# Performance work log

Measured on AMD Instinct MI355X. Metric: run time of the kernel, lower is better.

## Reference

```python
import jax, jax.numpy as jnp
import numpy as np

B, H, W, DIM = 8, 128, 128, 96
MED = 2 * DIM            # med_channels
NS = 3                   # num_scales
SCTX = 48                # spatial context channels
RIN = DIM + SCTX         # reweight mlp input
RHID = int(0.25 * RIN)   # 36
ROUT = NS * MED          # 576
FH, FWH = H, W // 2 + 1  # rfft2 output grid
SCALE_HW = [(16, 9), (8, 4), (24, 13)]  # per-scale filter resolutions


def _cubic(t, a=-0.75):
    t = abs(t)
    if t <= 1.0:
        return (a + 2) * t ** 3 - (a + 3) * t ** 2 + 1.0
    if t < 2.0:
        return a * t ** 3 - 5 * a * t ** 2 + 8 * a * t - 4 * a
    return 0.0


def _resize_mat(old, new):
    # bicubic, align_corners=True, border replication (matches F.interpolate)
    M = np.zeros((new, old), dtype=np.float32)
    for j in range(new):
        s = j * (old - 1) / (new - 1) if new > 1 else 0.0
        f = int(np.floor(s))
        for k in range(-1, 3):
            M[j, min(max(f + k, 0), old - 1)] += _cubic(s - (f + k))
    return jnp.asarray(M)


def _soa(x, scale, bias):
    r = jnp.maximum(x, 0.0)
    return scale * r * r + bias


def setup_inputs() -> dict:
    key = jax.random.key(0)
    ks = jax.random.split(key, 10)
    inp = {
        "x": jax.random.normal(ks[0], (B, H, W, DIM), dtype=jnp.float32),
        "w1": jax.random.normal(ks[1], (MED, DIM), dtype=jnp.float32) * 0.02,
        "soa1_scale": jnp.ones((1,), jnp.float32),
        "soa1_bias": jnp.zeros((1,), jnp.float32),
        "cw0": jax.random.normal(ks[2], (SCALE_HW[0][0], SCALE_HW[0][1], MED, 2), dtype=jnp.float32) * 0.02,
        "cw1": jax.random.normal(ks[3], (SCALE_HW[1][0], SCALE_HW[1][1], MED, 2), dtype=jnp.float32) * 0.02,
        "cw2": jax.random.normal(ks[4], (SCALE_HW[2][0], SCALE_HW[2][1], MED, 2), dtype=jnp.float32) * 0.02,
        "sp_w": jax.random.normal(ks[5], (SCTX, DIM), dtype=jnp.float32) * 0.05,
        "bn_gamma": jnp.ones((SCTX,), jnp.float32),
        "bn_beta": jnp.zeros((SCTX,), jnp.float32),
        "bn_mean": jnp.zeros((SCTX,), jnp.float32),
        "bn_var": jnp.ones((SCTX,), jnp.float32),
        "fc1": jax.random.normal(ks[6], (RHID, RIN), dtype=jnp.float32) * 0.05,
        "mlp_scale": jnp.ones((1,), jnp.float32),
        "mlp_bias": jnp.zeros((1,), jnp.float32),
        "fc2": jax.random.normal(ks[7], (ROUT, RHID), dtype=jnp.float32) * 0.05,
        "w2": jax.random.normal(ks[8], (DIM, MED), dtype=jnp.float32) * 0.02,
    }
    return inp


def reference(x, w1, soa1_scale, soa1_bias, cw0, cw1, cw2, sp_w,
              bn_gamma, bn_beta, bn_mean, bn_var,
              fc1, mlp_scale, mlp_bias, fc2, w2):
    # pwconv1 + Soa act
    x_pre = _soa(jnp.einsum('bhwc,mc->bhwm', x, w1), soa1_scale, soa1_bias)
    # rfft2 over spatial dims (ortho) -> [B, FH, FWH, MED] complex64
    xf = jnp.fft.rfft2(x_pre.transpose(0, 3, 1, 2), axes=(2, 3), norm='ortho').transpose(0, 2, 3, 1)
    # resize each scale's complex weight to the fft grid (bicubic align_corners=True)
    filts = []
    for cw in (cw0, cw1, cw2):
        Rh = _resize_mat(cw.shape[0], FH)
        Rw = _resize_mat(cw.shape[1], FWH)
        t = jnp.einsum('Hh,hwmc->Hwmc', Rh, cw)
        t = jnp.einsum('Ww,Hwmc->HWmc', Rw, t)
        filts.append(jax.lax.complex(t[..., 0], t[..., 1]))
    filt = jnp.stack(filts)  # [NS, FH, FWH, MED] complex64
    # routing context: global channel mean + 1x1 conv / BN(eval) / relu / GAP
    gctx = x.mean(axis=(1, 2))  # [B, DIM]
    y = jnp.einsum('bhwc,sc->bhws', x, sp_w)
    y = (y - bn_mean) * jax.lax.rsqrt(bn_var + 1e-5) * bn_gamma + bn_beta
    sctx = jnp.maximum(y, 0.0).mean(axis=(1, 2))  # [B, SCTX]
    fused = jnp.concatenate([gctx, sctx], axis=1)  # [B, RIN]
    hmid = _soa(fused @ fc1.T, mlp_scale, mlp_bias)
    r = jax.nn.softmax((hmid @ fc2.T).reshape(-1, NS, MED), axis=1)  # [B, NS, MED]
    # routing-weighted combined filter + spectral multiply
    comb = jnp.einsum('shwm,bsm->bhwm', filt, r.astype(filt.dtype))
    xff = xf * comb
    xsp = jnp.fft.irfft2(xff.transpose(0, 3, 1, 2), s=(H, W), axes=(2, 3), norm='ortho').transpose(0, 2, 3, 1)
    # act2 is Identity; pwconv2
    return jnp.einsum('bhwm,cm->bhwc', xsp, w2)
```

## Files before the change

kernel.cpp:

```cpp
#include <hip/hip_runtime.h>
#include <math.h>

#define BB    8
#define HH    128
#define WW    128
#define DIM   96
#define MED   192
#define HWPX  16384
#define FWH   65
#define LSTR  67

#define P_OFF     0
#define P_SZ      (8*192*16384)
#define FILT_OFF  (P_OFF + P_SZ)
#define FILT_SZ   (3*192*128*65*2)
#define GS_OFF    (FILT_OFF + FILT_SZ)
#define SS_OFF    (GS_OFF + 768)
#define R_OFF     (SS_OFF + 384)
#define W1B_OFF   (R_OFF + 4608)
#define W2B_OFF   (W1B_OFF + 23040)

typedef __attribute__((ext_vector_type(8))) short short8_t;
typedef __attribute__((ext_vector_type(4))) float float4_t;

__device__ __forceinline__ unsigned short bf16_rne(float f){
  unsigned u = __float_as_uint(f);
  unsigned r = (u + 0x7FFFu + ((u>>16)&1u)) >> 16;
  return (unsigned short)r;
}
__device__ __forceinline__ float bf16_to_f(unsigned short h){
  return __uint_as_float(((unsigned)h) << 16);
}

__global__ __launch_bounds__(256) void k_prep(
    const float* __restrict__ w1, const float* __restrict__ sp_w,
    const float* __restrict__ w2,
    unsigned short* __restrict__ W1B, unsigned short* __restrict__ W2B)
{
  int tid = threadIdx.x + blockIdx.x*256;
  int nthr = 256*36;
  for (int i = tid; i < 2*3*15*512; i += nthr) {
    int j = i & 7, l = (i>>3) & 63;
    int nt = (i>>9) % 15, kc = ((i>>9)/15) % 3, term = i / (3*15*512);
    int r = nt*16 + (l&15);
    int c = kc*32 + (l>>4)*8 + j;
    float v = (r < 192) ? w1[r*96 + c] : sp_w[(r-192)*96 + c];
    unsigned short hi = bf16_rne(v);
    W1B[i] = (term==0) ? hi : bf16_rne(v - bf16_to_f(hi));
  }
  for (int i = tid; i < 2*6*6*512; i += nthr) {
    int j = i & 7, l = (i>>3) & 63;
    int nt = (i>>9) % 6, kc = ((i>>9)/6) % 6, term = i / (6*6*512);
    int cp = nt*16 + (l&15);
    int m  = kc*32 + (l>>4)*8 + j;
    float v = w2[cp*192 + m];
    unsigned short hi = bf16_rne(v);
    W2B[i] = (term==0) ? hi : bf16_rne(v - bf16_to_f(hi));
  }
}

__global__ __launch_bounds__(256) void k_pw1(
    const float* __restrict__ x, const unsigned short* __restrict__ W1B,
    const float* __restrict__ soa_scale, const float* __restrict__ soa_bias,
    const float* __restrict__ bn_gamma, const float* __restrict__ bn_beta,
    const float* __restrict__ bn_mean, const float* __restrict__ bn_var,
    float* __restrict__ P, float* __restrict__ gsum, float* __restrict__ ssum)
{
  __shared__ float red[4][144];
  __shared__ float bnA_s[48], bnB_s[48];
  int t = threadIdx.x;
  int lane = t & 63, wv = t >> 6;
  if (t < 48) {
    float a = bn_gamma[t] * rsqrtf(bn_var[t] + 1e-5f);
    bnA_s[t] = a; bnB_s[t] = bn_beta[t] - bn_mean[t]*a;
  }
  int px0 = blockIdx.x*64 + wv*16;
  int b = (blockIdx.x*64) >> 14;
  int pxl = px0 & 16383;
  int g = lane >> 4;

  float4_t acc[15];
  #pragma unroll
  for (int nt=0; nt<15; ++nt) acc[nt] = (float4_t){0.f,0.f,0.f,0.f};

  #pragma unroll
  for (int kc=0; kc<3; ++kc) {
    const float* xp = x + (size_t)(px0 + (lane&15))*96 + kc*32 + g*8;
    float4 v0 = *(const float4*)xp;
    float4 v1 = *(const float4*)(xp+4);
    float vv[8] = {v0.x,v0.y,v0.z,v0.w, v1.x,v1.y,v1.z,v1.w};
    #pragma unroll
    for (int j=0;j<8;j++){
      float s = vv[j];
      s += __shfl_xor(s, 1);
      s += __shfl_xor(s, 2);
      s += __shfl_xor(s, 4);
      s += __shfl_xor(s, 8);
      if ((lane & 15) == 0) red[wv][kc*32 + g*8 + j] = s;
    }
    short8_t Bh, Bl;
    #pragma unroll
    for (int j=0;j<8;j++){
      unsigned short h = bf16_rne(vv[j]);
      Bh[j] = (short)h;
      Bl[j] = (short)bf16_rne(vv[j] - bf16_to_f(h));
    }
    const short8_t* a_hi = (const short8_t*)(W1B + (size_t)(0*3+kc)*15*512) + lane;
    const short8_t* a_lo = (const short8_t*)(W1B + (size_t)(1*3+kc)*15*512) + lane;
    #pragma unroll
    for (int nt=0; nt<15; ++nt) {
      short8_t Ah = a_hi[nt*64];
      short8_t Al = a_lo[nt*64];
      acc[nt] = __builtin_amdgcn_mfma_f32_16x16x32_bf16(Ah, Bh, acc[nt], 0,0,0);
      acc[nt] = __builtin_amdgcn_mfma_f32_16x16x32_bf16(Ah, Bl, acc[nt], 0,0,0);
      acc[nt] = __builtin_amdgcn_mfma_f32_16x16x32_bf16(Al, Bh, acc[nt], 0,0,0);
    }
  }
  float sc = soa_scale[0], bi = soa_bias[0];
  #pragma unroll
  for (int nt=0; nt<12; ++nt) {
    #pragma unroll
    for (int q=0;q<4;q++){
      float d = acc[nt][q];
      float v = fmaxf(d, 0.f);
      d = sc*v*v + bi;
      int mp = nt*16 + g*4 + q;
      P[(size_t)(b*192 + mp)*HWPX + pxl + (lane&15)] = d;
    }
  }
  #pragma unroll
  for (int tile=0; tile<3; ++tile) {
    #pragma unroll
    for (int q=0;q<4;q++){
      int s = tile*16 + g*4 + q;
      float y = acc[12+tile][q];
      float v = fmaxf(bnA_s[s]*y + bnB_s[s], 0.f);
      v += __shfl_xor(v, 1);
      v += __shfl_xor(v, 2);
      v += __shfl_xor(v, 4);
      v += __shfl_xor(v, 8);
      if ((lane & 15) == 0) red[wv][96 + s] = v;
    }
  }
  __syncthreads();
  if (t < 144) {
    float s = red[0][t] + red[1][t] + red[2][t] + red[3][t];
    if (t < 96) atomicAdd(&gsum[b*96 + t], s);
    else        atomicAdd(&ssum[b*48 + (t-96)], s);
  }
}

__global__ __launch_bounds__(256) void k_pw2(
    const float* __restrict__ P, const unsigned short* __restrict__ W2B,
    float* __restrict__ out)
{
  int t = threadIdx.x;
  int lane = t & 63, wv = t >> 6;
  int px0 = blockIdx.x*64 + wv*16;
  int b = px0 >> 14;
  int pxl = px0 & 16383;

  float4_t acc[6];
  #pragma unroll
  for (int nt=0; nt<6; ++nt) acc[nt] = (float4_t){0.f,0.f,0.f,0.f};

  #pragma unroll
  for (int kc=0; kc<6; ++kc) {
    const float* ap = P + (size_t)(b*192 + kc*32 + (lane>>4)*8)*HWPX + pxl + (lane&15);
    short8_t Ah, Al;
    #pragma unroll
    for (int j=0;j<8;j++){
      float v = ap[(size_t)j*HWPX];
      unsigned short h = bf16_rne(v);
      Ah[j] = (short)h;
      Al[j] = (short)bf16_rne(v - bf16_to_f(h));
    }
    const short8_t* b_hi = (const short8_t*)(W2B + (size_t)(0*6+kc)*6*512) + lane;
    const short8_t* b_lo = (const short8_t*)(W2B + (size_t)(1*6+kc)*6*512) + lane;
    #pragma unroll
    for (int nt=0; nt<6; ++nt) {
      short8_t Bh = b_hi[nt*64];
      short8_t Bl = b_lo[nt*64];
      acc[nt] = __builtin_amdgcn_mfma_f32_16x16x32_bf16(Ah, Bh, acc[nt], 0,0,0);
      acc[nt] = __builtin_amdgcn_mfma_f32_16x16x32_bf16(Ah, Bl, acc[nt], 0,0,0);
      acc[nt] = __builtin_amdgcn_mfma_f32_16x16x32_bf16(Al, Bh, acc[nt], 0,0,0);
    }
  }
  #pragma unroll
  for (int nt=0; nt<6; ++nt) {
    #pragma unroll
    for (int q=0;q<4;q++){
      int px = px0 + (lane>>4)*4 + q;
      out[(size_t)px*96 + nt*16 + (lane&15)] = acc[nt][q];
    }
  }
}

__global__ __launch_bounds__(256) void k_route2(
    const float* __restrict__ gsum, const float* __restrict__ ssum,
    const float* __restrict__ fc1, const float* __restrict__ fc2,
    const float* __restrict__ mlp_scale, const float* __restrict__ mlp_bias,
    float* __restrict__ r_out)
{
  __shared__ float fused[144], hmid[36], rpre[576];
  int t = threadIdx.x, b = blockIdx.x;
  if (t < 96) fused[t] = gsum[b*96+t] * (1.f/16384.f);
  else if (t < 144) fused[t] = ssum[b*48 + (t-96)] * (1.f/16384.f);
  __syncthreads();
  if (t < 36) {
    float a = 0.f;
    for (int i=0;i<144;i++) a = fmaf(fused[i], fc1[t*144+i], a);
    float rr = fmaxf(a, 0.f);
    hmid[t] = mlp_scale[0]*rr*rr + mlp_bias[0];
  }
  __syncthreads();
  for (int o = t; o < 576; o += 256) {
    float a = 0.f;
    for (int j=0;j<36;j++) a = fmaf(hmid[j], fc2[o*36+j], a);
    rpre[o] = a;
  }
  __syncthreads();
  if (t < 192) {
    float v0 = rpre[t], v1 = rpre[192+t], v2 = rpre[384+t];
    float mx = fmaxf(v0, fmaxf(v1, v2));
    float e0 = expf(v0-mx), e1 = expf(v1-mx), e2 = expf(v2-mx);
    float inv = 1.f/(e0+e1+e2);
    r_out[(b*3+0)*192+t] = e0*inv;
    r_out[(b*3+1)*192+t] = e1*inv;
    r_out[(b*3+2)*192+t] = e2*inv;
  }
}

__device__ __forceinline__ float cubicw(float tt){
  float t = fabsf(tt), t2=t*t, t3=t2*t;
  if (t <= 1.f) return 1.25f*t3 - 2.25f*t2 + 1.f;
  if (t < 2.f)  return -0.75f*t3 + 3.75f*t2 - 6.f*t + 3.f;
  return 0.f;
}

__global__ __launch_bounds__(256) void k_filt(
    const float* __restrict__ cw0, const float* __restrict__ cw1,
    const float* __restrict__ cw2, float* __restrict__ filt)
{
  int bx = blockIdx.x; int s = bx >> 7; int fh = bx & 127;
  const float* cw = (s==0) ? cw0 : ((s==1) ? cw1 : cw2);
  int SH = (s==0) ? 16 : ((s==1) ? 8 : 24);
  int SW = (s==0) ? 9  : ((s==1) ? 4 : 13);
  float sh = fh * (float)(SH-1) / 127.f;
  int fh0 = (int)floorf(sh);
  float wh[4]; int ih[4];
  #pragma unroll
  for (int k=0;k<4;k++){
    int kk = fh0-1+k;
    wh[k] = cubicw(sh - (float)kk);
    ih[k] = min(max(kk,0), SH-1);
  }
  int t = threadIdx.x;
  for (int i = t; i < 192*65; i += 256) {
    int m = i / 65, fw = i % 65;
    float sw = fw * (float)(SW-1) / 64.f;
    int fw0 = (int)floorf(sw);
    float are=0.f, aim=0.f;
    #pragma unroll
    for (int kb=0;kb<4;kb++){
      int jj = fw0-1+kb;
      float wwb = cubicw(sw - (float)jj);
      int iw = min(max(jj,0), SW-1);
      #pragma unroll
      for (int ka=0;ka<4;ka++){
        const float* p = cw + (size_t)((ih[ka]*SW + iw)*192 + m)*2;
        float wgt = wh[ka]*wwb;
        are = fmaf(wgt, p[0], are);
        aim = fmaf(wgt, p[1], aim);
      }
    }
    *(float2*)&filt[ (size_t)(((s*192+m)*128 + fh)*65 + fw) * 2 ] = make_float2(are, aim);
  }
}

__device__ __forceinline__ float2 c_add(float2 a, float2 b){ return make_float2(a.x+b.x, a.y+b.y); }
__device__ __forceinline__ float2 c_sub(float2 a, float2 b){ return make_float2(a.x-b.x, a.y-b.y); }
__device__ __forceinline__ float2 c_mul(float2 a, float2 w){ return make_float2(a.x*w.x - a.y*w.y, a.x*w.y + a.y*w.x); }
__device__ __forceinline__ float2 c_mulc(float2 a, float2 w){ return make_float2(a.x*w.x + a.y*w.y, a.y*w.x - a.x*w.y); }

__device__ __forceinline__ void dif4(float2* S, const float2* TW,
    int a0, int a1, int a2, int a3, int t1, int t2, int t3)
{
  float2 x0=S[a0], x1=S[a1], x2=S[a2], x3=S[a3];
  float2 u = c_add(x0,x2), d0 = c_sub(x0,x2);
  float2 s = c_add(x1,x3), d1 = c_sub(x1,x3);
  float2 w = c_mul(d0, TW[t1]);
  float2 v = c_mul(d1, TW[t2]);
  float2 t3w = TW[t3];
  S[a0] = c_add(u,s);
  S[a1] = c_mul(c_sub(u,s), t3w);
  S[a2] = c_add(w,v);
  S[a3] = c_mul(c_sub(w,v), t3w);
}

__device__ __forceinline__ void dit4(float2* S, const float2* TW,
    int a0, int a1, int a2, int a3, int tA, int tB, int tC)
{
  float2 x0=S[a0], x1=S[a1], x2=S[a2], x3=S[a3];
  float2 wA = TW[tA];
  float2 x1t = c_mulc(x1, wA), x3t = c_mulc(x3, wA);
  float2 u = c_add(x0,x1t), v = c_sub(x0,x1t);
  float2 s = c_add(x2,x3t), w = c_sub(x2,x3t);
  float2 st = c_mulc(s, TW[tB]);
  float2 wt = c_mulc(w, TW[tC]);
  S[a0] = c_add(u, st);
  S[a2] = c_sub(u, st);
  S[a1] = c_add(v, wt);
  S[a3] = c_sub(v, wt);
}

__global__ __launch_bounds__(512, 4) void k_spectral(
    float* __restrict__ P, const float* __restrict__ filt, const float* __restrict__ r)
{
  __shared__ float2 S[128*LSTR];
  __shared__ float2 TW[64];
  int t = threadIdx.x;
  int lane = t & 63, wid = t >> 6;

  int i = blockIdx.x;
  int b = (i >> 3) & 7;
  int m = (i & 7) * 24 + (i >> 6);
  float* plane = P + ((size_t)b*192 + m) * HWPX;

  {
    float ang = -6.283185307179586477f * (float)lane / 128.f;
    TW[lane] = make_float2(cosf(ang), sinf(ang));
  }

  for (int it = 0; it < 8; ++it) {
    int row = 4*wid + (lane>>4) + 32*(it>>1);
    int j   = (it&1)*16 + (lane&15);
    float4 v = ((const float4*)plane)[row*32 + j];
    int base = row*LSTR + 2*j;
    S[base]   = make_float2(v.x, v.y);
    S[base+1] = make_float2(v.z, v.w);
  }
  float r0 = r[(b*3+0)*192+m];
  float r1 = r[(b*3+1)*192+m];
  float r2 = r[(b*3+2)*192+m];

  #pragma unroll
  for (int ps = 0; ps < 3; ++ps) {
    const int lh = 5 - 2*ps;
    const int h1 = 1 << lh, h2 = h1 >> 1;
    #pragma unroll
    for (int it = 0; it < 4; ++it) {
      int g = lane & 15;
      int row = 4*wid + (lane>>4) + 32*it;
      int k = g & (h2-1), blk = g >> (lh-1);
      int base = row*LSTR + blk*(2*h1) + k;
      dif4(S,TW, base, base+h2, base+h1, base+h1+h2,
           k << (6-lh), (k+h2) << (6-lh), k << (7-lh));
    }
  }

  for (int it = 0; it < 9; ++it) {
    int loc = lane + 64*it;
    if (loc < 528) {
      int rl = loc / 33;
      int k  = loc - 33*rl;
      int row = 4*wid + (rl&3) + 32*(rl>>2);
      int base = row*LSTR;
      if (k == 0) {
        float2 z = S[base];
        S[base]    = make_float2(z.x + z.y, 0.f);
        S[base+64] = make_float2(z.x - z.y, 0.f);
      } else {
        int a = __brev((unsigned)k) >> 26;
        int bidx = __brev((unsigned)(64-k)) >> 26;
        float2 A = S[base+a], B = S[base+bidx];
        float sr_ = 0.5f*(A.x+B.x), si_ = 0.5f*(A.y-B.y);
        float dr  = 0.5f*(A.x-B.x), di  = 0.5f*(A.y+B.y);
        float2 wq = TW[k];
        float tr = wq.x*di + wq.y*dr;
        float ti = -(wq.x*dr - wq.y*di);
        S[base+a]    = make_float2(sr_ + tr,  si_ + ti);
        S[base+bidx] = make_float2(sr_ - tr, -si_ + ti);
      }
    }
  }
  __syncthreads();

  #pragma unroll
  for (int ps = 0; ps < 3; ++ps) {
    const int lh = 6 - 2*ps;
    const int h1 = 1 << lh, h2 = h1 >> 1;
    for (int it = 0; it < 5; ++it) {
      int idx = t + 512*it;
      if (idx < 65*32) {
        int g = idx / 65, col = idx - g*65;
        int k = g & (h2-1), blk = g >> (lh-1);
        int p = blk*(2*h1) + k;
        dif4(S,TW, p*LSTR+col, (p+h2)*LSTR+col, (p+h1)*LSTR+col, (p+h1+h2)*LSTR+col,
             k << (6-lh), (k+h2) << (6-lh), k << (7-lh));
      }
    }
    __syncthreads();
  }

  {
    const float2* fb0 = (const float2*)filt + (size_t)(0*192+m)*8320;
    const float2* fb1 = (const float2*)filt + (size_t)(1*192+m)*8320;
    const float2* fb2 = (const float2*)filt + (size_t)(2*192+m)*8320;
    const float inv = 1.f/8192.f;
    for (int it = 0; it < 9; ++it) {
      int idx = t + 512*it;
      if (idx < 65*64) {
        int f = idx / 65, fw = idx - f*65;
        int j = __brev((unsigned)f) >> 26;
        int cc = (fw == 64) ? 64 : (__brev((unsigned)fw) >> 26);
        int a0 = (2*j)*LSTR + cc, a1 = a0 + LSTR;
        float2 u = S[a0], v = S[a1];
        float2 e = c_add(u,v), o = c_sub(u,v);
        float2 f00=fb0[idx],      f10=fb1[idx],      f20=fb2[idx];
        float2 f01=fb0[idx+4160], f11=fb1[idx+4160], f21=fb2[idx+4160];
        float cr0 = (r0*f00.x + r1*f10.x + r2*f20.x) * inv;
        float ci0 = (r0*f00.y + r1*f10.y + r2*f20.y) * inv;
        float cr1 = (r0*f01.x + r1*f11.x + r2*f21.x) * inv;
        float ci1 = (r0*f01.y + r1*f11.y + r2*f21.y) * inv;
        S[a0] = make_float2(e.x*cr0 - e.y*ci0, e.x*ci0 + e.y*cr0);
        S[a1] = make_float2(o.x*cr1 - o.y*ci1, o.x*ci1 + o.y*cr1);
      }
    }
  }
  __syncthreads();

  #pragma unroll
  for (int ps = 0; ps < 3; ++ps) {
    const int la = 2*ps;
    const int h = 1 << la;
    for (int it = 0; it < 5; ++it) {
      int idx = t + 512*it;
      if (idx < 65*32) {
        int g = idx / 65, col = idx - g*65;
        int k = g & (h-1), blk = g >> la;
        int p = blk*(4*h) + k;
        dit4(S,TW, p*LSTR+col, (p+h)*LSTR+col, (p+2*h)*LSTR+col, (p+3*h)*LSTR+col,
             k << (6-la), k << (5-la), (k+h) << (5-la));
      }
    }
    __syncthreads();
  }
  for (int it = 0; it < 9; ++it) {
    int idx = t + 512*it;
    if (idx < 65*64) {
      int k = idx / 65, col = idx - k*65;
      int a0 = k*LSTR + col, a1 = a0 + 64*LSTR;
      float2 u = S[a0], xv = S[a1];
      float2 xt = c_mulc(xv, TW[k]);
      S[a0] = c_add(u,xt); S[a1] = c_sub(u,xt);
    }
  }
  __syncthreads();

  for (int it = 0; it < 9; ++it) {
    int loc = lane + 64*it;
    if (loc < 528) {
      int rl = loc / 33;
      int k  = loc - 33*rl;
      int row = 4*wid + (rl&3) + 32*(rl>>2);
      int base = row*LSTR;
      if (k == 0) {
        float ar = S[base].x;
        float cr = S[base+64].x;
        S[base] = make_float2(0.5f*(ar+cr), 0.5f*(ar-cr));
      } else {
        int a = __brev((unsigned)k) >> 26;
        int bidx = __brev((unsigned)(64-k)) >> 26;
        float2 A = S[base+a], B = S[base+bidx];
        float sr_ = 0.5f*(A.x+B.x), si_ = 0.5f*(A.y-B.y);
        float dr  = 0.5f*(A.x-B.x), di  = 0.5f*(A.y+B.y);
        float2 wq = TW[k];
        float tr2 = wq.y*dr - wq.x*di;
        float ti2 = wq.x*dr + wq.y*di;
        S[base+a]    = make_float2(sr_ + tr2,  si_ + ti2);
        S[base+bidx] = make_float2(sr_ - tr2, -si_ + ti2);
      }
    }
  }

  #pragma unroll
  for (int ps = 0; ps < 3; ++ps) {
    const int la = 2*ps;
    const int h = 1 << la;
    #pragma unroll
    for (int it = 0; it < 4; ++it) {
      int g = lane & 15;
      int row = 4*wid + (lane>>4) + 32*it;
      int k = g & (h-1), blk = g >> la;
      int base = row*LSTR + blk*(4*h) + k;
      dit4(S,TW, base, base+h, base+2*h, base+3*h,
           k << (6-la), k << (5-la), (k+h) << (5-la));
    }
  }

  for (int it = 0; it < 8; ++it) {
    int row = 4*wid + (lane>>4) + 32*(it>>1);
    int j   = (it&1)*16 + (lane&15);
    int base = row*LSTR + 2*j;
    float2 z0 = S[base], z1 = S[base+1];
    float4 v; v.x = z0.x; v.y = z0.y; v.z = z1.x; v.w = z1.y;
    ((float4*)plane)[row*32 + j] = v;
  }
}

extern "C" void kernel_launch(void* const* d_in, const int* in_sizes, int n_in,
                              void* d_out, int out_size, void* d_ws, size_t ws_size,
                              hipStream_t stream) {
  const float* x          = (const float*)d_in[0];
  const float* w1         = (const float*)d_in[1];
  const float* soa1_scale = (const float*)d_in[2];
  const float* soa1_bias  = (const float*)d_in[3];
  const float* cw0        = (const float*)d_in[4];
  const float* cw1        = (const float*)d_in[5];
  const float* cw2        = (const float*)d_in[6];
  const float* sp_w       = (const float*)d_in[7];
  const float* bn_gamma   = (const float*)d_in[8];
  const float* bn_beta    = (const float*)d_in[9];
  const float* bn_mean    = (const float*)d_in[10];
  const float* bn_var     = (const float*)d_in[11];
  const float* fc1        = (const float*)d_in[12];
  const float* mlp_scale  = (const float*)d_in[13];
  const float* mlp_bias   = (const float*)d_in[14];
  const float* fc2        = (const float*)d_in[15];
  const float* w2         = (const float*)d_in[16];
  float* out = (float*)d_out;

  float* ws   = (float*)d_ws;
  float* P    = ws + P_OFF;
  float* filt = ws + FILT_OFF;
  float* gsum = ws + GS_OFF;
  float* ssum = ws + SS_OFF;
  float* rbuf = ws + R_OFF;
  unsigned short* W1B = (unsigned short*)(ws + W1B_OFF);
  unsigned short* W2B = (unsigned short*)(ws + W2B_OFF);

  hipMemsetAsync(gsum, 0, (768+384)*sizeof(float), stream);

  k_prep   <<<36,   256, 0, stream>>>(w1, sp_w, w2, W1B, W2B);
  k_pw1    <<<2048, 256, 0, stream>>>(x, W1B, soa1_scale, soa1_bias,
                                      bn_gamma, bn_beta, bn_mean, bn_var,
                                      P, gsum, ssum);
  k_route2 <<<8,    256, 0, stream>>>(gsum, ssum, fc1, fc2, mlp_scale, mlp_bias, rbuf);
  k_filt   <<<384,  256, 0, stream>>>(cw0, cw1, cw2, filt);
  k_spectral<<<1536,512, 0, stream>>>(P, filt, rbuf);
  k_pw2    <<<2048, 256, 0, stream>>>(P, W2B, out);
}
```

Measured before the change: 419.0 us.

## Make filter resize separable via shared memory and remap spectral row ownership

The bicubic filter kernel now runs one block per (scale, channel). It first resizes along H into a shared-memory table, then resizes along W from that table. This replaces the 16-tap 2D gather per output with two 4-tap passes and writes contiguous output. In the spectral kernel each wave now owns a contiguous band of 16 rows instead of strided rows, and the real-FFT post-processing loops index by (k,row) without divisions. This improves coalescing and likely keeps rows wave-local, at the cost of a different LDS access pattern.

```diff
diff --git a/kernel.cpp b/kernel.cpp
--- a/kernel.cpp
+++ b/kernel.cpp
@@ -242,39 +242,48 @@
     const float* __restrict__ cw0, const float* __restrict__ cw1,
     const float* __restrict__ cw2, float* __restrict__ filt)
 {
-  int bx = blockIdx.x; int s = bx >> 7; int fh = bx & 127;
+  int bx = blockIdx.x;
+  int s = bx / 192, m = bx - s*192;
   const float* cw = (s==0) ? cw0 : ((s==1) ? cw1 : cw2);
-  int SH = (s==0) ? 16 : ((s==1) ? 8 : 24);
-  int SW = (s==0) ? 9  : ((s==1) ? 4 : 13);
-  float sh = fh * (float)(SH-1) / 127.f;
-  int fh0 = (int)floorf(sh);
-  float wh[4]; int ih[4];
-  #pragma unroll
-  for (int k=0;k<4;k++){
-    int kk = fh0-1+k;
-    wh[k] = cubicw(sh - (float)kk);
-    ih[k] = min(max(kk,0), SH-1);
-  }
+  const int SH = (s==0) ? 16 : ((s==1) ? 8 : 24);
+  const int SW = (s==0) ? 9  : ((s==1) ? 4 : 13);
+  __shared__ float2 T[128][13];
   int t = threadIdx.x;
-  for (int i = t; i < 192*65; i += 256) {
-    int m = i / 65, fw = i % 65;
+
+  for (int i = t; i < 128*SW; i += 256) {
+    int fh = i / SW, iw = i - fh*SW;
+    float sh = fh * (float)(SH-1) / 127.f;
+    int fh0 = (int)floorf(sh);
+    float2 acc = make_float2(0.f, 0.f);
+    #pragma unroll
+    for (int ka=0; ka<4; ++ka) {
+      int kk = fh0-1+ka;
+      float w = cubicw(sh - (float)kk);
+      int ih = min(max(kk,0), SH-1);
+      float2 v = *(const float2*)(cw + (size_t)((ih*SW + iw)*192 + m)*2);
+      acc.x = fmaf(w, v.x, acc.x);
+      acc.y = fmaf(w, v.y, acc.y);
+    }
+    T[fh][iw] = acc;
+  }
+  __syncthreads();
+
+  float2* outp = (float2*)filt + (size_t)(s*192+m)*8320;
+  for (int i = t; i < 128*65; i += 256) {
+    int fh = i / 65, fw = i - fh*65;
     float sw = fw * (float)(SW-1) / 64.f;
     int fw0 = (int)floorf(sw);
-    float are=0.f, aim=0.f;
-    #pragma unroll
-    for (int kb=0;kb<4;kb++){
+    float2 acc = make_float2(0.f, 0.f);
+    #pragma unroll
+    for (int kb=0; kb<4; ++kb) {
       int jj = fw0-1+kb;
-      float wwb = cubicw(sw - (float)jj);
+      float w = cubicw(sw - (float)jj);
       int iw = min(max(jj,0), SW-1);
-      #pragma unroll
-      for (int ka=0;ka<4;ka++){
-        const float* p = cw + (size_t)((ih[ka]*SW + iw)*192 + m)*2;
-        float wgt = wh[ka]*wwb;
-        are = fmaf(wgt, p[0], are);
-        aim = fmaf(wgt, p[1], aim);
-      }
-    }
-    *(float2*)&filt[ (size_t)(((s*192+m)*128 + fh)*65 + fw) * 2 ] = make_float2(are, aim);
+      float2 v = T[fh][iw];
+      acc.x = fmaf(w, v.x, acc.x);
+      acc.y = fmaf(w, v.y, acc.y);
+    }
+    outp[i] = acc;
   }
 }
 
@@ -333,8 +342,8 @@
   }
 
   for (int it = 0; it < 8; ++it) {
-    int row = 4*wid + (lane>>4) + 32*(it>>1);
-    int j   = (it&1)*16 + (lane&15);
+    int row = 16*wid + (lane>>5) + 2*it;
+    int j   = lane & 31;
     float4 v = ((const float4*)plane)[row*32 + j];
     int base = row*LSTR + 2*j;
     S[base]   = make_float2(v.x, v.y);
@@ -351,7 +360,7 @@
     #pragma unroll
     for (int it = 0; it < 4; ++it) {
       int g = lane & 15;
-      int row = 4*wid + (lane>>4) + 32*it;
+      int row = 16*wid + (lane>>4) + 4*it;
       int k = g & (h2-1), blk = g >> (lh-1);
       int base = row*LSTR + blk*(2*h1) + k;
       dif4(S,TW, base, base+h2, base+h1, base+h1+h2,
@@ -360,11 +369,9 @@
   }
 
   for (int it = 0; it < 9; ++it) {
-    int loc = lane + 64*it;
-    if (loc < 528) {
-      int rl = loc / 33;
-      int k  = loc - 33*rl;
-      int row = 4*wid + (rl&3) + 32*(rl>>2);
+    int k   = (lane>>4) + 4*it;
+    int row = 16*wid + (lane & 15);
+    if (k <= 32) {
       int base = row*LSTR;
       if (k == 0) {
         float2 z = S[base];
@@ -459,11 +466,9 @@
   __syncthreads();
 
   for (int it = 0; it < 9; ++it) {
-    int loc = lane + 64*it;
-    if (loc < 528) {
-      int rl = loc / 33;
-      int k  = loc - 33*rl;
-      int row = 4*wid + (rl&3) + 32*(rl>>2);
+    int k   = (lane>>4) + 4*it;
+    int row = 16*wid + (lane & 15);
+    if (k <= 32) {
       int base = row*LSTR;
       if (k == 0) {
         float ar = S[base].x;
@@ -491,7 +496,7 @@
     #pragma unroll
     for (int it = 0; it < 4; ++it) {
       int g = lane & 15;
-      int row = 4*wid + (lane>>4) + 32*it;
+      int row = 16*wid + (lane>>4) + 4*it;
       int k = g & (h-1), blk = g >> la;
       int base = row*LSTR + blk*(4*h) + k;
       dit4(S,TW, base, base+h, base+2*h, base+3*h,
@@ -500,8 +505,8 @@
   }
 
   for (int it = 0; it < 8; ++it) {
-    int row = 4*wid + (lane>>4) + 32*(it>>1);
-    int j   = (it&1)*16 + (lane&15);
+    int row = 16*wid + (lane>>5) + 2*it;
+    int j   = lane & 31;
     int base = row*LSTR + 2*j;
     float2 z0 = S[base], z1 = S[base+1];
     float4 v; v.x = z0.x; v.y = z0.y; v.z = z1.x; v.w = z1.y;
@@ -547,7 +552,7 @@
                                       bn_gamma, bn_beta, bn_mean, bn_var,
                                       P, gsum, ssum);
   k_route2 <<<8,    256, 0, stream>>>(gsum, ssum, fc1, fc2, mlp_scale, mlp_bias, rbuf);
-  k_filt   <<<384,  256, 0, stream>>>(cw0, cw1, cw2, filt);
+  k_filt   <<<576,  256, 0, stream>>>(cw0, cw1, cw2, filt);
   k_spectral<<<1536,512, 0, stream>>>(P, filt, rbuf);
   k_pw2    <<<2048, 256, 0, stream>>>(P, W2B, out);
 }
```

New measurement: 365.9 us. 12.7% less time.
